# Optimization experiments

Measured on AMD Instinct MI355X. Metric: run time of the kernel, lower is better.

The kernel has to match this reference:

```python
import jax, jax.numpy as jnp
import numpy as np
from jax import lax

EPS = 1e-5
NUM_GROUPS = 4  # min(4, output_channels)


def setup_inputs() -> dict:
    key = jax.random.key(0)
    ks = jax.random.split(key, 8)
    B, C, T, H, W = 8, 64, 16, 56, 56
    Cout = 128
    return {
        "x": jax.random.normal(ks[0], (B, C, T, H, W), jnp.float32),
        "spatial_w": jax.random.normal(ks[1], (C, 1, 3, 3), jnp.float32) * 0.1,
        "spatial_b": jax.random.normal(ks[2], (C,), jnp.float32) * 0.1,
        "temporal_w": jax.random.normal(ks[3], (C, 1, 3, 1, 1), jnp.float32) * 0.1,
        "temporal_b": jax.random.normal(ks[4], (C,), jnp.float32) * 0.1,
        "pointwise_w": jax.random.normal(ks[5], (Cout, C), jnp.float32) * 0.1,
        "pointwise_b": jax.random.normal(ks[6], (Cout,), jnp.float32) * 0.1,
        "gn_w": jnp.ones((Cout,), jnp.float32),
        "gn_b": jnp.zeros((Cout,), jnp.float32),
    }


def reference(x, spatial_w, spatial_b, temporal_w, temporal_b,
              pointwise_w, pointwise_b, gn_w, gn_b):
    B, C, T, H, W = x.shape
    Cout = pointwise_w.shape[0]

    # Depthwise spatial conv2d: batch the per-frame loop by folding T into N.
    xs = x.transpose(0, 2, 1, 3, 4).reshape(B * T, C, H, W)
    ys = lax.conv_general_dilated(
        xs, spatial_w, window_strides=(1, 1), padding=((1, 1), (1, 1)),
        dimension_numbers=("NCHW", "OIHW", "NCHW"), feature_group_count=C)
    ys = ys + spatial_b[None, :, None, None]
    y = ys.reshape(B, T, C, H, W).transpose(0, 2, 1, 3, 4)  # (B,C,T,H,W)

    # Depthwise temporal conv3d with kernel (3,1,1), padding (1,0,0).
    z = lax.conv_general_dilated(
        y, temporal_w, window_strides=(1, 1, 1),
        padding=((1, 1), (0, 0), (0, 0)),
        dimension_numbers=("NCDHW", "OIDHW", "NCDHW"), feature_group_count=C)
    z = z + temporal_b[None, :, None, None, None]

    # Pointwise 1x1x1 conv == channel GEMM.
    p = jnp.einsum("bcthw,oc->bothw", z, pointwise_w)
    p = p + pointwise_b[None, :, None, None, None]

    # GroupNorm (num_groups=4) + ReLU.
    pg = p.reshape(B, NUM_GROUPS, Cout // NUM_GROUPS, T, H, W)
    mean = pg.mean(axis=(2, 3, 4, 5), keepdims=True)
    var = pg.var(axis=(2, 3, 4, 5), keepdims=True)
    normed = ((pg - mean) * lax.rsqrt(var + EPS)).reshape(B, Cout, T, H, W)
    out = normed * gn_w[None, :, None, None, None] + gn_b[None, :, None, None, None]
    return jax.nn.relu(out)
```

## Files before the change

kernel.cpp:

```cpp
#include <hip/hip_runtime.h>
#include <hip/hip_bf16.h>

#define Bb 8
#define Cc 64
#define Tt 16
#define Hh 56
#define Ww 56
#define COUT 128
#define HW (Hh*Ww)
#define THW (Tt*HW)
#define NPG ((double)(32*THW))

typedef __attribute__((ext_vector_type(8))) short short8v;
typedef __attribute__((ext_vector_type(4))) float f32x4;

__device__ __forceinline__ unsigned short f2bf(float x) {
  __hip_bfloat16 h = __float2bfloat16(x);
  return *reinterpret_cast<unsigned short*>(&h);
}
__device__ __forceinline__ float blo(unsigned int u) {
  return __uint_as_float(u << 16);
}
__device__ __forceinline__ float bhi(unsigned int u) {
  return __uint_as_float(u & 0xFFFF0000u);
}
__device__ __forceinline__ unsigned int pack2(float a, float b) {
  return (unsigned int)f2bf(a) | ((unsigned int)f2bf(b) << 16);
}

__global__ __launch_bounds__(256) void k1_dwconv(
    const float* __restrict__ x,  const float* __restrict__ sw,
    const float* __restrict__ sb, const float* __restrict__ tw,
    const float* __restrict__ tb, unsigned int* __restrict__ zq,
    double* __restrict__ stats)
{
  __shared__ unsigned int raw[HW];
  __shared__ unsigned int ring[3][HW];

  const int tid = threadIdx.x;
  if (blockIdx.x == 0 && tid < 64) stats[tid] = 0.0;

  const int tq = blockIdx.x & 3;
  const int c2 = (blockIdx.x >> 2) & 31;
  const int b  =  blockIdx.x >> 7;
  const int t0 = tq * 4;
  const int ca = c2 * 2, cb = ca + 1;

  float s9a[9], s9b[9];
#pragma unroll
  for (int k = 0; k < 9; ++k) { s9a[k] = sw[ca * 9 + k]; s9b[k] = sw[cb * 9 + k]; }
  float ta3[3], tb3[3];
#pragma unroll
  for (int k = 0; k < 3; ++k) { ta3[k] = tw[ca * 3 + k]; tb3[k] = tw[cb * 3 + k]; }
  const float sba = sb[ca], sbb = sb[cb];
  const float tba = tb[ca], tbb = tb[cb];

  const float* xa = x + (size_t)(b * Cc + ca) * THW;
  const float* xb = x + (size_t)(b * Cc + cb) * THW;
  unsigned int* zbase = zq + (size_t)(b * 32 + c2) * THW;

  for (int tt = t0 - 1; tt <= t0 + 4; ++tt) {
    if (tt >= 0 && tt < Tt) {
      const float* xpa = xa + tt * HW;
      const float* xpb = xb + tt * HW;
      for (int f = tid; f < HW / 4; f += 256) {
        float4 va = *(const float4*)(xpa + f * 4);
        float4 vb = *(const float4*)(xpb + f * 4);
        uint4 pk;
        pk.x = pack2(va.x, vb.x);
        pk.y = pack2(va.y, vb.y);
        pk.z = pack2(va.z, vb.z);
        pk.w = pack2(va.w, vb.w);
        *(uint4*)&raw[f * 4] = pk;
      }
    }
    __syncthreads();

    if (tt >= 0 && tt < Tt) {
      unsigned int* rg = ring[tt % 3];
      for (int q = tid; q < HW / 4; q += 256) {
        int h  = q / 14;
        int w0 = (q - h * 14) * 4;
        float sa0 = sba, sa1 = sba, sa2 = sba, sa3 = sba;
        float sb0 = sbb, sb1 = sbb, sb2 = sbb, sb3 = sbb;
#pragma unroll
        for (int dh = -1; dh <= 1; ++dh) {
          int hh = h + dh;
          if (hh < 0 || hh > Hh - 1) continue;
          const unsigned int* rr = &raw[hh * Ww + w0];
          uint4 mv = *(const uint4*)rr;
          unsigned int lf = (w0 > 0)      ? rr[-1] : 0u;
          unsigned int rt = (w0 < Ww - 4) ? rr[4]  : 0u;
          float am1 = blo(lf),  a0 = blo(mv.x), a1 = blo(mv.y);
          float a2  = blo(mv.z), a3 = blo(mv.w), a4 = blo(rt);
          float bm1 = bhi(lf),  b0 = bhi(mv.x), b1 = bhi(mv.y);
          float b2  = bhi(mv.z), b3 = bhi(mv.w), b4 = bhi(rt);
          float k0a = s9a[(dh + 1) * 3 + 0], k1a = s9a[(dh + 1) * 3 + 1], k2a = s9a[(dh + 1) * 3 + 2];
          float k0b = s9b[(dh + 1) * 3 + 0], k1b = s9b[(dh + 1) * 3 + 1], k2b = s9b[(dh + 1) * 3 + 2];
          sa0 = fmaf(k0a, am1, fmaf(k1a, a0, fmaf(k2a, a1, sa0)));
          sa1 = fmaf(k0a, a0,  fmaf(k1a, a1, fmaf(k2a, a2, sa1)));
          sa2 = fmaf(k0a, a1,  fmaf(k1a, a2, fmaf(k2a, a3, sa2)));
          sa3 = fmaf(k0a, a2,  fmaf(k1a, a3, fmaf(k2a, a4, sa3)));
          sb0 = fmaf(k0b, bm1, fmaf(k1b, b0, fmaf(k2b, b1, sb0)));
          sb1 = fmaf(k0b, b0,  fmaf(k1b, b1, fmaf(k2b, b2, sb1)));
          sb2 = fmaf(k0b, b1,  fmaf(k1b, b2, fmaf(k2b, b3, sb2)));
          sb3 = fmaf(k0b, b2,  fmaf(k1b, b3, fmaf(k2b, b4, sb3)));
        }
        uint4 pk;
        pk.x = pack2(sa0, sb0);
        pk.y = pack2(sa1, sb1);
        pk.z = pack2(sa2, sb2);
        pk.w = pack2(sa3, sb3);
        *(uint4*)&rg[q * 4] = pk;
      }
    }
    __syncthreads();

    int t_out = tt - 1;
    if (t_out >= t0 && t_out <= t0 + 3) {
      unsigned int* zp = zbase + (size_t)t_out * HW;
      for (int q = tid; q < HW / 4; q += 256) {
        float aa0 = tba, aa1 = tba, aa2 = tba, aa3 = tba;
        float bb0 = tbb, bb1 = tbb, bb2 = tbb, bb3 = tbb;
#pragma unroll
        for (int dt = -1; dt <= 1; ++dt) {
          int ti = t_out + dt;
          if (ti < 0 || ti > Tt - 1) continue;
          float tka = ta3[dt + 1], tkb = tb3[dt + 1];
          uint4 v = *(const uint4*)&ring[ti % 3][q * 4];
          aa0 = fmaf(tka, blo(v.x), aa0);  bb0 = fmaf(tkb, bhi(v.x), bb0);
          aa1 = fmaf(tka, blo(v.y), aa1);  bb1 = fmaf(tkb, bhi(v.y), bb1);
          aa2 = fmaf(tka, blo(v.z), aa2);  bb2 = fmaf(tkb, bhi(v.z), bb2);
          aa3 = fmaf(tka, blo(v.w), aa3);  bb3 = fmaf(tkb, bhi(v.w), bb3);
        }
        uint4 o;
        o.x = pack2(aa0, bb0);
        o.y = pack2(aa1, bb1);
        o.z = pack2(aa2, bb2);
        o.w = pack2(aa3, bb3);
        *(uint4*)(zp + q * 4) = o;
      }
    }
    __syncthreads();
  }
}

#define WFRAG_LOAD()                                                           \
  const int lr = tid & 15, lg = (tid >> 4) & 3, wv = tid >> 6;                 \
  const int obase = wv * 32;                                                   \
  short8v wfrag[2][2];                                                         \
  _Pragma("unroll")                                                            \
  for (int ot = 0; ot < 2; ++ot)                                               \
    _Pragma("unroll")                                                          \
    for (int kt = 0; kt < 2; ++kt) {                                           \
      int o  = obase + ot * 16 + lr;                                           \
      int c0 = kt * 32 + lg * 8;                                               \
      float4 wa = *(const float4*)(pw + o * 64 + c0);                          \
      float4 wb = *(const float4*)(pw + o * 64 + c0 + 4);                      \
      short8v fr;                                                              \
      fr[0] = (short)f2bf(wa.x); fr[1] = (short)f2bf(wa.y);                    \
      fr[2] = (short)f2bf(wa.z); fr[3] = (short)f2bf(wa.w);                    \
      fr[4] = (short)f2bf(wb.x); fr[5] = (short)f2bf(wb.y);                    \
      fr[6] = (short)f2bf(wb.z); fr[7] = (short)f2bf(wb.w);                    \
      wfrag[ot][kt] = fr;                                                      \
    }

#define LDR(it) {                                                              \
  int p0 = (it) * 128;                                                         \
  _Pragma("unroll")                                                            \
  for (int i = 0; i < 4; ++i) {                                                \
    int f = tid + i * 256; int c2r = f >> 5; int po = (f & 31) << 2;           \
    st[i] = *(const uint4*)(zb + (size_t)c2r * THW + p0 + po);                 \
  } }

#define STL(bf) {                                                              \
  _Pragma("unroll")                                                            \
  for (int i = 0; i < 4; ++i) {                                                \
    int f = tid + i * 256; int c2r = f >> 5; int po = (f & 31) << 2;           \
    *(uint4*)&zt[bf][c2r * 132 + po] = st[i];                                  \
  } }

#define MFMA_TILE(bufidx)                                                      \
  f32x4 acc[2][8];                                                             \
  _Pragma("unroll")                                                            \
  for (int ot = 0; ot < 2; ++ot)                                               \
    _Pragma("unroll")                                                          \
    for (int pt = 0; pt < 8; ++pt) {                                           \
      acc[ot][pt][0] = 0.f; acc[ot][pt][1] = 0.f;                              \
      acc[ot][pt][2] = 0.f; acc[ot][pt][3] = 0.f;                              \
    }                                                                          \
  {                                                                            \
    const unsigned int* ztc = zt[bufidx];                                      \
    _Pragma("unroll")                                                          \
    for (int kt = 0; kt < 2; ++kt) {                                           \
      const int c2b = kt * 16 + lg * 4;                                        \
      _Pragma("unroll")                                                        \
      for (int pt = 0; pt < 8; ++pt) {                                         \
        const unsigned int* zp2 = &ztc[c2b * 132 + pt * 16 + lr];              \
        union { unsigned int u[4]; short8v s; } zfu;                           \
        zfu.u[0] = zp2[0];   zfu.u[1] = zp2[132];                              \
        zfu.u[2] = zp2[264]; zfu.u[3] = zp2[396];                              \
        acc[0][pt] = __builtin_amdgcn_mfma_f32_16x16x32_bf16(                  \
            zfu.s, wfrag[0][kt], acc[0][pt], 0, 0, 0);                         \
        acc[1][pt] = __builtin_amdgcn_mfma_f32_16x16x32_bf16(                  \
            zfu.s, wfrag[1][kt], acc[1][pt], 0, 0, 0);                         \
      }                                                                        \
    }                                                                          \
  }

__global__ __launch_bounds__(256) void k2_stats(
    const unsigned int* __restrict__ zq, const float* __restrict__ pw,
    const float* __restrict__ pb, double* __restrict__ stats)
{
  __shared__ unsigned int zt[2][32 * 132];
  const int tid = threadIdx.x;
  const int b  = blockIdx.x / 98;
  const int pg = blockIdx.x - b * 98;

  WFRAG_LOAD();

  const float pbl[2] = { pb[obase + lr], pb[obase + 16 + lr] };

  const unsigned int* zb = zq + (size_t)(b * 32) * THW + pg * 512;

  uint4 st[4];
  LDR(0); STL(0);

  float s1 = 0.0f, s2 = 0.0f;
  for (int it = 0; it < 4; ++it) {
    __syncthreads();
    if (it < 3) LDR(it + 1);
    MFMA_TILE(it & 1);
    if (it < 3) STL((it + 1) & 1);
#pragma unroll
    for (int ot = 0; ot < 2; ++ot)
#pragma unroll
      for (int pt = 0; pt < 8; ++pt)
#pragma unroll
        for (int r = 0; r < 4; ++r) {
          float d = acc[ot][pt][r] + pbl[ot];
          s1 += d;
          s2 = fmaf(d, d, s2);
        }
  }

#pragma unroll
  for (int off = 32; off; off >>= 1) {
    s1 += __shfl_xor(s1, off);
    s2 += __shfl_xor(s2, off);
  }
  if ((tid & 63) == 0) {
    atomicAdd(&stats[(b * 4 + wv) * 2 + 0], (double)s1);
    atomicAdd(&stats[(b * 4 + wv) * 2 + 1], (double)s2);
  }
}

__global__ __launch_bounds__(256) void k3_norm(
    const unsigned int* __restrict__ zq, const float* __restrict__ pw,
    const float* __restrict__ pb, const double* __restrict__ stats,
    const float* __restrict__ gnw, const float* __restrict__ gnb,
    float* __restrict__ out)
{
  __shared__ unsigned int zt[2][32 * 132];
  const int tid = threadIdx.x;
  const int b  = blockIdx.x / 98;
  const int pg = blockIdx.x - b * 98;

  WFRAG_LOAD();

  double sm1 = stats[(b * 4 + wv) * 2 + 0];
  double sm2 = stats[(b * 4 + wv) * 2 + 1];
  double md = sm1 / NPG;
  double vd = sm2 / NPG - md * md;
  float m   = (float)md;
  float inv = rsqrtf((float)vd + 1e-5f);

  float Ac[2], Bc[2];
#pragma unroll
  for (int ot = 0; ot < 2; ++ot) {
    int o = obase + ot * 16 + lr;
    float A = inv * gnw[o];
    Ac[ot] = A;
    Bc[ot] = fmaf(pb[o] - m, A, gnb[o]);
  }

  const unsigned int* zb = zq + (size_t)(b * 32) * THW + pg * 512;
  float* ob = out + (size_t)(b * COUT) * THW + pg * 512 + lg * 4;

  uint4 st[4];
  LDR(0); STL(0);

  for (int it = 0; it < 4; ++it) {
    __syncthreads();
    if (it < 3) LDR(it + 1);
    MFMA_TILE(it & 1);
    if (it < 3) STL((it + 1) & 1);
#pragma unroll
    for (int ot = 0; ot < 2; ++ot) {
      int o = obase + ot * 16 + lr;
      float A = Ac[ot], B = Bc[ot];
      float* orow = ob + (size_t)o * THW + it * 128;
#pragma unroll
      for (int pt = 0; pt < 8; ++pt) {
        f32x4 a = acc[ot][pt];
        float4 v;
        v.x = fmaf(a[0], A, B); v.x = v.x > 0.0f ? v.x : 0.0f;
        v.y = fmaf(a[1], A, B); v.y = v.y > 0.0f ? v.y : 0.0f;
        v.z = fmaf(a[2], A, B); v.z = v.z > 0.0f ? v.z : 0.0f;
        v.w = fmaf(a[3], A, B); v.w = v.w > 0.0f ? v.w : 0.0f;
        *(float4*)(orow + pt * 16) = v;
      }
    }
  }
}

extern "C" void kernel_launch(void* const* d_in, const int* in_sizes, int n_in,
                              void* d_out, int out_size, void* d_ws, size_t ws_size,
                              hipStream_t stream)
{
  const float* x   = (const float*)d_in[0];
  const float* sw  = (const float*)d_in[1];
  const float* sb  = (const float*)d_in[2];
  const float* tw  = (const float*)d_in[3];
  const float* tb  = (const float*)d_in[4];
  const float* pw  = (const float*)d_in[5];
  const float* pb  = (const float*)d_in[6];
  const float* gnw = (const float*)d_in[7];
  const float* gnb = (const float*)d_in[8];
  float* out = (float*)d_out;

  double* stats    = (double*)d_ws;
  unsigned int* zq = (unsigned int*)((char*)d_ws + 512);

  k1_dwconv<<<Bb * 32 * 4, 256, 0, stream>>>(x, sw, sb, tw, tb, zq, stats);
  k2_stats<<<Bb * 98, 256, 0, stream>>>(zq, pw, pb, stats);
  k3_norm <<<Bb * 98, 256, 0, stream>>>(zq, pw, pb, stats, gnw, gnb, out);
}
```

Before: 169.0 us.

## Fuse stats and normalize kernels with a grid-wide atomic barrier

Merges the GroupNorm statistics pass and the normalize/ReLU pass into one persistent kernel of 392 blocks. Each block handles two pixel tiles and accumulates stats, then waits on a global atomic counter barrier before reading the final stats and recomputing the GEMM to write output. This removes one kernel launch and the tail/launch gap between passes. In exchange it relies on all 392 blocks being co-resident (launch bounds of 2 blocks per CU), which risks deadlock if occupancy is lower, and it halves the block count, which lowers parallelism.

```diff
diff --git a/kernel.cpp b/kernel.cpp
--- a/kernel.cpp
+++ b/kernel.cpp
@@ -10,6 +10,7 @@
 #define HW (Hh*Ww)
 #define THW (Tt*HW)
 #define NPG ((double)(32*THW))
+#define NBLK23 392u
 
 typedef __attribute__((ext_vector_type(8))) short short8v;
 typedef __attribute__((ext_vector_type(4))) float f32x4;
@@ -32,13 +33,16 @@
     const float* __restrict__ x,  const float* __restrict__ sw,
     const float* __restrict__ sb, const float* __restrict__ tw,
     const float* __restrict__ tb, unsigned int* __restrict__ zq,
-    double* __restrict__ stats)
+    double* __restrict__ stats, unsigned int* __restrict__ ctr)
 {
   __shared__ unsigned int raw[HW];
   __shared__ unsigned int ring[3][HW];
 
   const int tid = threadIdx.x;
-  if (blockIdx.x == 0 && tid < 64) stats[tid] = 0.0;
+  if (blockIdx.x == 0) {
+    if (tid < 64) stats[tid] = 0.0;
+    if (tid == 64) *ctr = 0u;
+  }
 
   const int tq = blockIdx.x & 3;
   const int c2 = (blockIdx.x >> 2) & 31;
@@ -208,68 +212,71 @@
     }                                                                          \
   }
 
-__global__ __launch_bounds__(256) void k2_stats(
+__global__ __launch_bounds__(256, 2) void k23_fused(
     const unsigned int* __restrict__ zq, const float* __restrict__ pw,
-    const float* __restrict__ pb, double* __restrict__ stats)
-{
-  __shared__ unsigned int zt[2][32 * 132];
-  const int tid = threadIdx.x;
-  const int b  = blockIdx.x / 98;
-  const int pg = blockIdx.x - b * 98;
-
-  WFRAG_LOAD();
-
-  const float pbl[2] = { pb[obase + lr], pb[obase + 16 + lr] };
-
-  const unsigned int* zb = zq + (size_t)(b * 32) * THW + pg * 512;
-
-  uint4 st[4];
-  LDR(0); STL(0);
-
-  float s1 = 0.0f, s2 = 0.0f;
-  for (int it = 0; it < 4; ++it) {
-    __syncthreads();
-    if (it < 3) LDR(it + 1);
-    MFMA_TILE(it & 1);
-    if (it < 3) STL((it + 1) & 1);
-#pragma unroll
-    for (int ot = 0; ot < 2; ++ot)
-#pragma unroll
-      for (int pt = 0; pt < 8; ++pt)
-#pragma unroll
-        for (int r = 0; r < 4; ++r) {
-          float d = acc[ot][pt][r] + pbl[ot];
-          s1 += d;
-          s2 = fmaf(d, d, s2);
-        }
-  }
-
-#pragma unroll
-  for (int off = 32; off; off >>= 1) {
-    s1 += __shfl_xor(s1, off);
-    s2 += __shfl_xor(s2, off);
-  }
-  if ((tid & 63) == 0) {
-    atomicAdd(&stats[(b * 4 + wv) * 2 + 0], (double)s1);
-    atomicAdd(&stats[(b * 4 + wv) * 2 + 1], (double)s2);
-  }
-}
-
-__global__ __launch_bounds__(256) void k3_norm(
-    const unsigned int* __restrict__ zq, const float* __restrict__ pw,
-    const float* __restrict__ pb, const double* __restrict__ stats,
+    const float* __restrict__ pb, double* __restrict__ stats,
+    unsigned int* __restrict__ ctr,
     const float* __restrict__ gnw, const float* __restrict__ gnb,
     float* __restrict__ out)
 {
   __shared__ unsigned int zt[2][32 * 132];
   const int tid = threadIdx.x;
-  const int b  = blockIdx.x / 98;
-  const int pg = blockIdx.x - b * 98;
+  const int tile0 = blockIdx.x * 2;
+  const int b   = tile0 / 98;
+  const int pg0 = tile0 - b * 98;
 
   WFRAG_LOAD();
-
-  double sm1 = stats[(b * 4 + wv) * 2 + 0];
-  double sm2 = stats[(b * 4 + wv) * 2 + 1];
+  const float pbl[2] = { pb[obase + lr], pb[obase + 16 + lr] };
+
+  uint4 st[4];
+
+  float s1 = 0.0f, s2 = 0.0f;
+  for (int j = 0; j < 2; ++j) {
+    const unsigned int* zb = zq + (size_t)(b * 32) * THW + (pg0 + j) * 512;
+    LDR(0); STL(0);
+    for (int it = 0; it < 4; ++it) {
+      __syncthreads();
+      if (it < 3) LDR(it + 1);
+      MFMA_TILE(it & 1);
+      if (it < 3) STL((it + 1) & 1);
+#pragma unroll
+      for (int ot = 0; ot < 2; ++ot)
+#pragma unroll
+        for (int pt = 0; pt < 8; ++pt)
+#pragma unroll
+          for (int r = 0; r < 4; ++r) {
+            float d = acc[ot][pt][r] + pbl[ot];
+            s1 += d;
+            s2 = fmaf(d, d, s2);
+          }
+    }
+    __syncthreads();
+  }
+#pragma unroll
+  for (int off = 32; off; off >>= 1) {
+    s1 += __shfl_xor(s1, off);
+    s2 += __shfl_xor(s2, off);
+  }
+  if ((tid & 63) == 0) {
+    atomicAdd(&stats[(b * 4 + wv) * 2 + 0], (double)s1);
+    atomicAdd(&stats[(b * 4 + wv) * 2 + 1], (double)s2);
+  }
+
+  __syncthreads();
+  if (tid == 0) {
+    __threadfence();
+    atomicAdd(ctr, 1u);
+    while (__hip_atomic_load(ctr, __ATOMIC_ACQUIRE, __HIP_MEMORY_SCOPE_AGENT)
+           < NBLK23) {
+      __builtin_amdgcn_s_sleep(32);
+    }
+  }
+  __syncthreads();
+
+  double sm1 = __hip_atomic_load(&stats[(b * 4 + wv) * 2 + 0],
+                                 __ATOMIC_ACQUIRE, __HIP_MEMORY_SCOPE_AGENT);
+  double sm2 = __hip_atomic_load(&stats[(b * 4 + wv) * 2 + 1],
+                                 __ATOMIC_ACQUIRE, __HIP_MEMORY_SCOPE_AGENT);
   double md = sm1 / NPG;
   double vd = sm2 / NPG - md * md;
   float m   = (float)md;
@@ -284,33 +291,33 @@
     Bc[ot] = fmaf(pb[o] - m, A, gnb[o]);
   }
 
-  const unsigned int* zb = zq + (size_t)(b * 32) * THW + pg * 512;
-  float* ob = out + (size_t)(b * COUT) * THW + pg * 512 + lg * 4;
-
-  uint4 st[4];
-  LDR(0); STL(0);
-
-  for (int it = 0; it < 4; ++it) {
-    __syncthreads();
-    if (it < 3) LDR(it + 1);
-    MFMA_TILE(it & 1);
-    if (it < 3) STL((it + 1) & 1);
-#pragma unroll
-    for (int ot = 0; ot < 2; ++ot) {
-      int o = obase + ot * 16 + lr;
-      float A = Ac[ot], B = Bc[ot];
-      float* orow = ob + (size_t)o * THW + it * 128;
-#pragma unroll
-      for (int pt = 0; pt < 8; ++pt) {
-        f32x4 a = acc[ot][pt];
-        float4 v;
-        v.x = fmaf(a[0], A, B); v.x = v.x > 0.0f ? v.x : 0.0f;
-        v.y = fmaf(a[1], A, B); v.y = v.y > 0.0f ? v.y : 0.0f;
-        v.z = fmaf(a[2], A, B); v.z = v.z > 0.0f ? v.z : 0.0f;
-        v.w = fmaf(a[3], A, B); v.w = v.w > 0.0f ? v.w : 0.0f;
-        *(float4*)(orow + pt * 16) = v;
+  for (int j = 0; j < 2; ++j) {
+    const unsigned int* zb = zq + (size_t)(b * 32) * THW + (pg0 + j) * 512;
+    float* ob = out + (size_t)(b * COUT) * THW + (pg0 + j) * 512 + lg * 4;
+    LDR(0); STL(0);
+    for (int it = 0; it < 4; ++it) {
+      __syncthreads();
+      if (it < 3) LDR(it + 1);
+      MFMA_TILE(it & 1);
+      if (it < 3) STL((it + 1) & 1);
+#pragma unroll
+      for (int ot = 0; ot < 2; ++ot) {
+        int o = obase + ot * 16 + lr;
+        float A = Ac[ot], B = Bc[ot];
+        float* orow = ob + (size_t)o * THW + it * 128;
+#pragma unroll
+        for (int pt = 0; pt < 8; ++pt) {
+          f32x4 a = acc[ot][pt];
+          float4 v;
+          v.x = fmaf(a[0], A, B); v.x = v.x > 0.0f ? v.x : 0.0f;
+          v.y = fmaf(a[1], A, B); v.y = v.y > 0.0f ? v.y : 0.0f;
+          v.z = fmaf(a[2], A, B); v.z = v.z > 0.0f ? v.z : 0.0f;
+          v.w = fmaf(a[3], A, B); v.w = v.w > 0.0f ? v.w : 0.0f;
+          *(float4*)(orow + pt * 16) = v;
+        }
       }
     }
+    __syncthreads();
   }
 }
 
@@ -329,10 +336,10 @@
   const float* gnb = (const float*)d_in[8];
   float* out = (float*)d_out;
 
-  double* stats    = (double*)d_ws;
-  unsigned int* zq = (unsigned int*)((char*)d_ws + 512);
-
-  k1_dwconv<<<Bb * 32 * 4, 256, 0, stream>>>(x, sw, sb, tw, tb, zq, stats);
-  k2_stats<<<Bb * 98, 256, 0, stream>>>(zq, pw, pb, stats);
-  k3_norm <<<Bb * 98, 256, 0, stream>>>(zq, pw, pb, stats, gnw, gnb, out);
-}
+  double* stats     = (double*)d_ws;
+  unsigned int* ctr = (unsigned int*)((char*)d_ws + 512);
+  unsigned int* zq  = (unsigned int*)((char*)d_ws + 1024);
+
+  k1_dwconv<<<Bb * 32 * 4, 256, 0, stream>>>(x, sw, sb, tw, tb, zq, stats, ctr);
+  k23_fused<<<NBLK23, 256, 0, stream>>>(zq, pw, pb, stats, ctr, gnw, gnb, out);
+}
```

Result: slower. 200.7 us (+18.8%).

## Software-pipeline global loads in depthwise conv and GEMM kernels with register prefetch

Applied to the files above, without the earlier changes.

In the depthwise conv kernel, the next frame's x planes are loaded into registers while the current frame is converted and convolved, and the trailing barrier per frame is removed. In the stats and norm kernels, the 4-iteration loop is fully unrolled so global loads run two tiles ahead of the MFMA work through two register staging sets. The aim is to hide global memory latency behind compute. The cost is higher register pressure, and dropping the end-of-iteration barrier relies on the raw buffer writes being ordered by the remaining barriers.

```diff
diff --git a/kernel.cpp b/kernel.cpp
--- a/kernel.cpp
+++ b/kernel.cpp
@@ -59,24 +59,54 @@
   const float* xb = x + (size_t)(b * Cc + cb) * THW;
   unsigned int* zbase = zq + (size_t)(b * 32 + c2) * THW;
 
-  for (int tt = t0 - 1; tt <= t0 + 4; ++tt) {
-    if (tt >= 0 && tt < Tt) {
-      const float* xpa = xa + tt * HW;
-      const float* xpb = xb + tt * HW;
-      for (int f = tid; f < HW / 4; f += 256) {
-        float4 va = *(const float4*)(xpa + f * 4);
-        float4 vb = *(const float4*)(xpb + f * 4);
-        uint4 pk;
-        pk.x = pack2(va.x, vb.x);
-        pk.y = pack2(va.y, vb.y);
-        pk.z = pack2(va.z, vb.z);
-        pk.w = pack2(va.w, vb.w);
-        *(uint4*)&raw[f * 4] = pk;
-      }
+  float4 pA[4], pB[4], qA[4], qB[4];
+
+#define LOADP(TT, RA, RB) {                                                    \
+    int _t = (TT);                                                             \
+    if (_t >= 0 && _t < Tt && _t <= t0 + 4) {                                  \
+      const float* _xa = xa + _t * HW;                                         \
+      const float* _xb = xb + _t * HW;                                         \
+      _Pragma("unroll")                                                        \
+      for (int i = 0; i < 4; ++i) {                                            \
+        int f = tid + i * 256;                                                 \
+        if (f < HW / 4) {                                                      \
+          RA[i] = *(const float4*)(_xa + f * 4);                               \
+          RB[i] = *(const float4*)(_xb + f * 4);                               \
+        }                                                                      \
+      }                                                                        \
+    } }
+
+#define RAWW(RA, RB) {                                                         \
+    _Pragma("unroll")                                                          \
+    for (int i = 0; i < 4; ++i) {                                              \
+      int f = tid + i * 256;                                                   \
+      if (f < HW / 4) {                                                        \
+        uint4 pk;                                                              \
+        pk.x = pack2(RA[i].x, RB[i].x);                                        \
+        pk.y = pack2(RA[i].y, RB[i].y);                                        \
+        pk.z = pack2(RA[i].z, RB[i].z);                                        \
+        pk.w = pack2(RA[i].w, RB[i].w);                                        \
+        *(uint4*)&raw[f * 4] = pk;                                             \
+      }                                                                        \
+    } }
+
+  LOADP(t0 - 1, pA, pB);
+
+#pragma unroll
+  for (int k = 0; k < 6; ++k) {
+    const int tt = t0 - 1 + k;
+    const bool val = (tt >= 0 && tt < Tt);
+
+    if (k & 1) {
+      if (val) RAWW(qA, qB);
+      LOADP(tt + 1, pA, pB);
+    } else {
+      if (val) RAWW(pA, pB);
+      LOADP(tt + 1, qA, qB);
     }
     __syncthreads();
 
-    if (tt >= 0 && tt < Tt) {
+    if (val) {
       unsigned int* rg = ring[tt % 3];
       for (int q = tid; q < HW / 4; q += 256) {
         int h  = q / 14;
@@ -116,7 +146,7 @@
     }
     __syncthreads();
 
-    int t_out = tt - 1;
+    const int t_out = tt - 1;
     if (t_out >= t0 && t_out <= t0 + 3) {
       unsigned int* zp = zbase + (size_t)t_out * HW;
       for (int q = tid; q < HW / 4; q += 256) {
@@ -141,8 +171,9 @@
         *(uint4*)(zp + q * 4) = o;
       }
     }
-    __syncthreads();
-  }
+  }
+#undef LOADP
+#undef RAWW
 }
 
 #define WFRAG_LOAD()                                                           \
@@ -165,19 +196,19 @@
       wfrag[ot][kt] = fr;                                                      \
     }
 
-#define LDR(it) {                                                              \
+#define LDRV(it, S) {                                                          \
   int p0 = (it) * 128;                                                         \
   _Pragma("unroll")                                                            \
   for (int i = 0; i < 4; ++i) {                                                \
     int f = tid + i * 256; int c2r = f >> 5; int po = (f & 31) << 2;           \
-    st[i] = *(const uint4*)(zb + (size_t)c2r * THW + p0 + po);                 \
+    S[i] = *(const uint4*)(zb + (size_t)c2r * THW + p0 + po);                  \
   } }
 
-#define STL(bf) {                                                              \
+#define STLV(S, bf) {                                                          \
   _Pragma("unroll")                                                            \
   for (int i = 0; i < 4; ++i) {                                                \
     int f = tid + i * 256; int c2r = f >> 5; int po = (f & 31) << 2;           \
-    *(uint4*)&zt[bf][c2r * 132 + po] = st[i];                                  \
+    *(uint4*)&zt[bf][c2r * 132 + po] = S[i];                                   \
   } }
 
 #define MFMA_TILE(bufidx)                                                      \
@@ -208,6 +239,18 @@
     }                                                                          \
   }
 
+#define STATS_BODY()                                                           \
+  _Pragma("unroll")                                                            \
+  for (int ot = 0; ot < 2; ++ot)                                               \
+    _Pragma("unroll")                                                          \
+    for (int pt = 0; pt < 8; ++pt)                                             \
+      _Pragma("unroll")                                                        \
+      for (int r = 0; r < 4; ++r) {                                            \
+        float d = acc[ot][pt][r] + pbl[ot];                                    \
+        s1 += d;                                                               \
+        s2 = fmaf(d, d, s2);                                                   \
+      }
+
 __global__ __launch_bounds__(256) void k2_stats(
     const unsigned int* __restrict__ zq, const float* __restrict__ pw,
     const float* __restrict__ pb, double* __restrict__ stats)
@@ -218,31 +261,23 @@
   const int pg = blockIdx.x - b * 98;
 
   WFRAG_LOAD();
-
   const float pbl[2] = { pb[obase + lr], pb[obase + 16 + lr] };
-
   const unsigned int* zb = zq + (size_t)(b * 32) * THW + pg * 512;
 
-  uint4 st[4];
-  LDR(0); STL(0);
+  uint4 sA[4], sB[4];
+  LDRV(0, sA); STLV(sA, 0); LDRV(1, sB);
 
   float s1 = 0.0f, s2 = 0.0f;
-  for (int it = 0; it < 4; ++it) {
-    __syncthreads();
-    if (it < 3) LDR(it + 1);
-    MFMA_TILE(it & 1);
-    if (it < 3) STL((it + 1) & 1);
-#pragma unroll
-    for (int ot = 0; ot < 2; ++ot)
-#pragma unroll
-      for (int pt = 0; pt < 8; ++pt)
-#pragma unroll
-        for (int r = 0; r < 4; ++r) {
-          float d = acc[ot][pt][r] + pbl[ot];
-          s1 += d;
-          s2 = fmaf(d, d, s2);
-        }
-  }
+  __syncthreads();
+  LDRV(2, sA);
+  { MFMA_TILE(0); STLV(sB, 1); STATS_BODY(); }
+  __syncthreads();
+  LDRV(3, sB);
+  { MFMA_TILE(1); STLV(sA, 0); STATS_BODY(); }
+  __syncthreads();
+  { MFMA_TILE(0); STLV(sB, 1); STATS_BODY(); }
+  __syncthreads();
+  { MFMA_TILE(1); STATS_BODY(); }
 
 #pragma unroll
   for (int off = 32; off; off >>= 1) {
@@ -254,6 +289,24 @@
     atomicAdd(&stats[(b * 4 + wv) * 2 + 1], (double)s2);
   }
 }
+
+#define STORE_BODY(itn)                                                        \
+  _Pragma("unroll")                                                            \
+  for (int ot = 0; ot < 2; ++ot) {                                             \
+    int o = obase + ot * 16 + lr;                                              \
+    float A = Ac[ot], B = Bc[ot];                                              \
+    float* orow = ob + (size_t)o * THW + (itn) * 128;                          \
+    _Pragma("unroll")                                                          \
+    for (int pt = 0; pt < 8; ++pt) {                                           \
+      f32x4 a = acc[ot][pt];                                                   \
+      float4 v;                                                                \
+      v.x = fmaf(a[0], A, B); v.x = v.x > 0.0f ? v.x : 0.0f;                   \
+      v.y = fmaf(a[1], A, B); v.y = v.y > 0.0f ? v.y : 0.0f;                   \
+      v.z = fmaf(a[2], A, B); v.z = v.z > 0.0f ? v.z : 0.0f;                   \
+      v.w = fmaf(a[3], A, B); v.w = v.w > 0.0f ? v.w : 0.0f;                   \
+      *(float4*)(orow + pt * 16) = v;                                          \
+    }                                                                          \
+  }
 
 __global__ __launch_bounds__(256) void k3_norm(
     const unsigned int* __restrict__ zq, const float* __restrict__ pw,
@@ -287,31 +340,19 @@
   const unsigned int* zb = zq + (size_t)(b * 32) * THW + pg * 512;
   float* ob = out + (size_t)(b * COUT) * THW + pg * 512 + lg * 4;
 
-  uint4 st[4];
-  LDR(0); STL(0);
-
-  for (int it = 0; it < 4; ++it) {
-    __syncthreads();
-    if (it < 3) LDR(it + 1);
-    MFMA_TILE(it & 1);
-    if (it < 3) STL((it + 1) & 1);
-#pragma unroll
-    for (int ot = 0; ot < 2; ++ot) {
-      int o = obase + ot * 16 + lr;
-      float A = Ac[ot], B = Bc[ot];
-      float* orow = ob + (size_t)o * THW + it * 128;
-#pragma unroll
-      for (int pt = 0; pt < 8; ++pt) {
-        f32x4 a = acc[ot][pt];
-        float4 v;
-        v.x = fmaf(a[0], A, B); v.x = v.x > 0.0f ? v.x : 0.0f;
-        v.y = fmaf(a[1], A, B); v.y = v.y > 0.0f ? v.y : 0.0f;
-        v.z = fmaf(a[2], A, B); v.z = v.z > 0.0f ? v.z : 0.0f;
-        v.w = fmaf(a[3], A, B); v.w = v.w > 0.0f ? v.w : 0.0f;
-        *(float4*)(orow + pt * 16) = v;
-      }
-    }
-  }
+  uint4 sA[4], sB[4];
+  LDRV(0, sA); STLV(sA, 0); LDRV(1, sB);
+
+  __syncthreads();
+  LDRV(2, sA);
+  { MFMA_TILE(0); STLV(sB, 1); STORE_BODY(0); }
+  __syncthreads();
+  LDRV(3, sB);
+  { MFMA_TILE(1); STLV(sA, 0); STORE_BODY(1); }
+  __syncthreads();
+  { MFMA_TILE(0); STLV(sB, 1); STORE_BODY(2); }
+  __syncthreads();
+  { MFMA_TILE(1); STORE_BODY(3); }
 }
 
 extern "C" void kernel_launch(void* const* d_in, const int* in_sizes, int n_in,
```

Result: slower. 173.7 us (+2.8%).
